# Performance work log

Measured on AMD Instinct MI355X. Metric: run time of the kernel, lower is better.

The kernel has to match this reference:

```python
import jax, jax.numpy as jnp
import numpy as np

EMBED = 4
H1, H2 = 8, 4


def setup_inputs() -> dict:
    key = jax.random.key(0)
    ks = jax.random.split(key, 10)
    x = jax.random.normal(ks[0], (1024, 256, EMBED), dtype=jnp.float32)
    Wq = jax.random.normal(ks[1], (EMBED, EMBED), dtype=jnp.float32)
    Wk = jax.random.normal(ks[2], (EMBED, EMBED), dtype=jnp.float32)
    Wv = jax.random.normal(ks[3], (EMBED, EMBED), dtype=jnp.float32)
    # nn.Linear default init: U(-1/sqrt(fan_in), 1/sqrt(fan_in)); approximate with uniform
    def lin(k, fan_in, fan_out):
        k1, k2 = jax.random.split(k)
        bound = 1.0 / np.sqrt(fan_in)
        W = jax.random.uniform(k1, (fan_in, fan_out), minval=-bound, maxval=bound, dtype=jnp.float32)
        b = jax.random.uniform(k2, (fan_out,), minval=-bound, maxval=bound, dtype=jnp.float32)
        return W, b
    W1, b1 = lin(ks[4], EMBED, H1)
    W2, b2 = lin(ks[5], H1, H2)
    W3, b3 = lin(ks[6], H2, 1)
    return {"x": x, "Wq": Wq, "Wk": Wk, "Wv": Wv,
            "W1": W1, "b1": b1, "W2": W2, "b2": b2, "W3": W3, "b3": b3}


def reference(x, Wq, Wk, Wv, W1, b1, W2, b2, W3, b3):
    # Self-attention: x [B, S, E]
    q = x @ Wq
    k = x @ Wk
    v = x @ Wv
    scale = 1.0 / np.sqrt(EMBED).astype(np.float32)
    scores = jax.nn.softmax(jnp.einsum('bse,bte->bst', q, k) * scale, axis=-1)
    attn_out = jnp.einsum('bst,bte->bse', scores, v)
    h = jnp.tanh(attn_out @ W1 + b1)
    h = jnp.tanh(h @ W2 + b2)
    return h @ W3 + b3  # [B, S, 1]
```

## Files before the change

kernel.cpp:

```cpp
#include <hip/hip_runtime.h>
#include <math.h>

constexpr int S  = 256;
constexpr int E  = 4;
constexpr int H1 = 8;
constexpr int H2 = 4;
constexpr int NW    = 4;
constexpr int CHUNK = S / NW;
constexpr int R     = 4;

__global__ __launch_bounds__(256, 4) void attn_mlp_kernel(
    const float* __restrict__ x,
    const float* __restrict__ Wq, const float* __restrict__ Wk, const float* __restrict__ Wv,
    const float* __restrict__ W1, const float* __restrict__ b1,
    const float* __restrict__ W2, const float* __restrict__ b2,
    const float* __restrict__ W3, const float* __restrict__ b3,
    float* __restrict__ out)
{
    const int b    = blockIdx.x;
    const int tid  = threadIdx.x;
    const int w    = tid >> 6;
    const int lane = tid & 63;

    __shared__ float4 q_lds[S];
    __shared__ float4 k_lds[S];
    __shared__ float4 v_lds[S];
    __shared__ float2 ml_lds[NW][S];
    __shared__ float4 acc_lds[NW][S];

    const float4 xr = *reinterpret_cast<const float4*>(x + ((size_t)b * S + tid) * E);
    const float xv[E] = {xr.x, xr.y, xr.z, xr.w};
    {
        float4 q, k, v;
        float* qp = &q.x; float* kp = &k.x; float* vp = &v.x;
        #pragma unroll
        for (int e = 0; e < E; ++e) {
            float aq = 0.f, ak = 0.f, av = 0.f;
            #pragma unroll
            for (int i = 0; i < E; ++i) {
                aq = fmaf(xv[i], Wq[i * E + e], aq);
                ak = fmaf(xv[i], Wk[i * E + e], ak);
                av = fmaf(xv[i], Wv[i * E + e], av);
            }
            qp[e] = aq * 0.5f;
            kp[e] = ak;
            vp[e] = av;
        }
        q_lds[tid] = q; k_lds[tid] = k; v_lds[tid] = v;
    }
    __syncthreads();

    const int j0 = w * CHUNK;
    float4 qr[R];
    #pragma unroll
    for (int rr = 0; rr < R; ++rr) qr[rr] = q_lds[lane + 64 * rr];

    float m[R];
    #pragma unroll
    for (int rr = 0; rr < R; ++rr) m[rr] = -3.0e38f;

    #pragma unroll 4
    for (int j = 0; j < CHUNK; ++j) {
        const float4 k = k_lds[j0 + j];
        #pragma unroll
        for (int rr = 0; rr < R; ++rr) {
            float s = qr[rr].x * k.x;
            s = fmaf(qr[rr].y, k.y, s);
            s = fmaf(qr[rr].z, k.z, s);
            s = fmaf(qr[rr].w, k.w, s);
            m[rr] = fmaxf(m[rr], s);
        }
    }

    float l[R];
    float4 acc[R];
    #pragma unroll
    for (int rr = 0; rr < R; ++rr) {
        l[rr] = 0.f;
        acc[rr] = make_float4(0.f, 0.f, 0.f, 0.f);
    }

    #pragma unroll 4
    for (int j = 0; j < CHUNK; ++j) {
        const float4 k = k_lds[j0 + j];
        const float4 v = v_lds[j0 + j];
        #pragma unroll
        for (int rr = 0; rr < R; ++rr) {
            float s = qr[rr].x * k.x;
            s = fmaf(qr[rr].y, k.y, s);
            s = fmaf(qr[rr].z, k.z, s);
            s = fmaf(qr[rr].w, k.w, s);
            const float p = __expf(s - m[rr]);
            l[rr] += p;
            acc[rr].x = fmaf(p, v.x, acc[rr].x);
            acc[rr].y = fmaf(p, v.y, acc[rr].y);
            acc[rr].z = fmaf(p, v.z, acc[rr].z);
            acc[rr].w = fmaf(p, v.w, acc[rr].w);
        }
    }

    #pragma unroll
    for (int rr = 0; rr < R; ++rr) {
        const int row = lane + 64 * rr;
        ml_lds[w][row]  = make_float2(m[rr], l[rr]);
        acc_lds[w][row] = acc[rr];
    }
    __syncthreads();

    float mstar = -3.0e38f;
    float2 mlw[NW];
    #pragma unroll
    for (int ww = 0; ww < NW; ++ww) {
        mlw[ww] = ml_lds[ww][tid];
        mstar = fmaxf(mstar, mlw[ww].x);
    }
    float lsum = 0.f;
    float ax = 0.f, ay = 0.f, az = 0.f, aw = 0.f;
    #pragma unroll
    for (int ww = 0; ww < NW; ++ww) {
        const float c = __expf(mlw[ww].x - mstar);
        lsum = fmaf(mlw[ww].y, c, lsum);
        const float4 a4 = acc_lds[ww][tid];
        ax = fmaf(a4.x, c, ax);
        ay = fmaf(a4.y, c, ay);
        az = fmaf(a4.z, c, az);
        aw = fmaf(a4.w, c, aw);
    }
    const float inv = 1.0f / lsum;
    const float a[E] = {ax * inv, ay * inv, az * inv, aw * inv};

    float h1[H1];
    #pragma unroll
    for (int o = 0; o < H1; ++o) {
        float s = b1[o];
        #pragma unroll
        for (int i = 0; i < E; ++i) s = fmaf(a[i], W1[i * H1 + o], s);
        h1[o] = tanhf(s);
    }
    float h2[H2];
    #pragma unroll
    for (int o = 0; o < H2; ++o) {
        float s = b2[o];
        #pragma unroll
        for (int i = 0; i < H1; ++i) s = fmaf(h1[i], W2[i * H2 + o], s);
        h2[o] = tanhf(s);
    }
    float r = b3[0];
    #pragma unroll
    for (int i = 0; i < H2; ++i) r = fmaf(h2[i], W3[i], r);

    out[(size_t)b * S + tid] = r;
}

extern "C" void kernel_launch(void* const* d_in, const int* in_sizes, int n_in,
                              void* d_out, int out_size, void* d_ws, size_t ws_size,
                              hipStream_t stream) {
    const float* x  = (const float*)d_in[0];
    const float* Wq = (const float*)d_in[1];
    const float* Wk = (const float*)d_in[2];
    const float* Wv = (const float*)d_in[3];
    const float* W1 = (const float*)d_in[4];
    const float* b1 = (const float*)d_in[5];
    const float* W2 = (const float*)d_in[6];
    const float* b2 = (const float*)d_in[7];
    const float* W3 = (const float*)d_in[8];
    const float* b3 = (const float*)d_in[9];
    float* out = (float*)d_out;

    const int B = in_sizes[0] / (S * E);
    attn_mlp_kernel<<<dim3(B), dim3(256), 0, stream>>>(
        x, Wq, Wk, Wv, W1, b1, W2, b2, W3, b3, out);
}
```

Baseline: 99.93 us.

## Replace softmax max pass with Cauchy-Schwarz bound and exp2 with folded log2e

Measured after the change: 94.87 us. 5.1% less time.

```diff
diff --git a/kernel.cpp b/kernel.cpp
--- a/kernel.cpp
+++ b/kernel.cpp
@@ -25,8 +25,9 @@
     __shared__ float4 q_lds[S];
     __shared__ float4 k_lds[S];
     __shared__ float4 v_lds[S];
-    __shared__ float2 ml_lds[NW][S];
     __shared__ float4 acc_lds[NW][S];
+    __shared__ float  l_lds[NW][S];
+    __shared__ float  kmax_lds[NW];
 
     const float4 xr = *reinterpret_cast<const float4*>(x + ((size_t)b * S + tid) * E);
     const float xv[E] = {xr.x, xr.y, xr.z, xr.w};
@@ -42,37 +43,36 @@
                 ak = fmaf(xv[i], Wk[i * E + e], ak);
                 av = fmaf(xv[i], Wv[i * E + e], av);
             }
-            qp[e] = aq * 0.5f;
+            qp[e] = aq * (0.5f * 1.44269504f);
             kp[e] = ak;
             vp[e] = av;
         }
         q_lds[tid] = q; k_lds[tid] = k; v_lds[tid] = v;
+
+        float kk = fmaf(k.x, k.x, fmaf(k.y, k.y, fmaf(k.z, k.z, k.w * k.w)));
+        #pragma unroll
+        for (int off = 32; off > 0; off >>= 1)
+            kk = fmaxf(kk, __shfl_xor(kk, off));
+        if (lane == 0) kmax_lds[w] = kk;
     }
     __syncthreads();
 
-    const int j0 = w * CHUNK;
+    const float kmax2 = fmaxf(fmaxf(kmax_lds[0], kmax_lds[1]),
+                              fmaxf(kmax_lds[2], kmax_lds[3]));
+
     float4 qr[R];
+    float  mh[R];
     #pragma unroll
-    for (int rr = 0; rr < R; ++rr) qr[rr] = q_lds[lane + 64 * rr];
-
-    float m[R];
-    #pragma unroll
-    for (int rr = 0; rr < R; ++rr) m[rr] = -3.0e38f;
-
-    #pragma unroll 4
-    for (int j = 0; j < CHUNK; ++j) {
-        const float4 k = k_lds[j0 + j];
-        #pragma unroll
-        for (int rr = 0; rr < R; ++rr) {
-            float s = qr[rr].x * k.x;
-            s = fmaf(qr[rr].y, k.y, s);
-            s = fmaf(qr[rr].z, k.z, s);
-            s = fmaf(qr[rr].w, k.w, s);
-            m[rr] = fmaxf(m[rr], s);
-        }
+    for (int rr = 0; rr < R; ++rr) {
+        qr[rr] = q_lds[lane + 64 * rr];
+        const float qq = fmaf(qr[rr].x, qr[rr].x,
+                          fmaf(qr[rr].y, qr[rr].y,
+                           fmaf(qr[rr].z, qr[rr].z, qr[rr].w * qr[rr].w)));
+        mh[rr] = sqrtf(qq * kmax2);
     }
 
-    float l[R];
+    const int j0 = w * CHUNK;
+    float  l[R];
     float4 acc[R];
     #pragma unroll
     for (int rr = 0; rr < R; ++rr) {
@@ -86,11 +86,11 @@
         const float4 v = v_lds[j0 + j];
         #pragma unroll
         for (int rr = 0; rr < R; ++rr) {
-            float s = qr[rr].x * k.x;
-            s = fmaf(qr[rr].y, k.y, s);
-            s = fmaf(qr[rr].z, k.z, s);
-            s = fmaf(qr[rr].w, k.w, s);
-            const float p = __expf(s - m[rr]);
+            float s = fmaf(qr[rr].x, k.x,
+                       fmaf(qr[rr].y, k.y,
+                        fmaf(qr[rr].z, k.z,
+                         fmaf(qr[rr].w, k.w, -mh[rr]))));
+            const float p = __builtin_amdgcn_exp2f(s);
             l[rr] += p;
             acc[rr].x = fmaf(p, v.x, acc[rr].x);
             acc[rr].y = fmaf(p, v.y, acc[rr].y);
@@ -102,29 +102,18 @@
     #pragma unroll
     for (int rr = 0; rr < R; ++rr) {
         const int row = lane + 64 * rr;
-        ml_lds[w][row]  = make_float2(m[rr], l[rr]);
         acc_lds[w][row] = acc[rr];
+        l_lds[w][row]   = l[rr];
     }
     __syncthreads();
 
-    float mstar = -3.0e38f;
-    float2 mlw[NW];
-    #pragma unroll
-    for (int ww = 0; ww < NW; ++ww) {
-        mlw[ww] = ml_lds[ww][tid];
-        mstar = fmaxf(mstar, mlw[ww].x);
-    }
     float lsum = 0.f;
     float ax = 0.f, ay = 0.f, az = 0.f, aw = 0.f;
     #pragma unroll
     for (int ww = 0; ww < NW; ++ww) {
-        const float c = __expf(mlw[ww].x - mstar);
-        lsum = fmaf(mlw[ww].y, c, lsum);
+        lsum += l_lds[ww][tid];
         const float4 a4 = acc_lds[ww][tid];
-        ax = fmaf(a4.x, c, ax);
-        ay = fmaf(a4.y, c, ay);
-        az = fmaf(a4.z, c, az);
-        aw = fmaf(a4.w, c, aw);
+        ax += a4.x; ay += a4.y; az += a4.z; aw += a4.w;
     }
     const float inv = 1.0f / lsum;
     const float a[E] = {ax * inv, ay * inv, az * inv, aw * inv};
```
